# Optimization experiments

Hardware: AMD Instinct MI355X
Metric: run time of the kernel (lower is better)

The kernel has to match this reference:

```python
import jax, jax.numpy as jnp
import numpy as np
import math

STD = math.exp(0.0025)  # exp(0.5 * 0.005) from log_sigma = 0.005
C = 0.5 * math.log(2 * math.pi)
B, X, H, Z, L, W = 8192, 512, 256, 64, 16, 32

def _predict(h, Wd, bd, Wo, bo):
    return jax.nn.sigmoid(jax.nn.relu(h @ Wd.T + bd) @ Wo.T + bo)

def _gru(xin, h, Wih, Whh, bih, bhh):
    gi = xin @ Wih.T + bih
    gh = h @ Whh.T + bhh
    ir, iz, inn = jnp.split(gi, 3, axis=1)
    hr, hz, hn = jnp.split(gh, 3, axis=1)
    r = jax.nn.sigmoid(ir + hr)
    zt = jax.nn.sigmoid(iz + hz)
    n = jnp.tanh(inn + r * hn)
    return (1.0 - zt) * n + zt * h

def setup_inputs():
    key = jax.random.key(0)
    ks = iter(jax.random.split(key, 40))
    def nrm(shape, s=0.05):
        return jax.random.normal(next(ks), shape, dtype=jnp.float32) * s
    return {
        "x": jax.random.uniform(next(ks), (B, X), dtype=jnp.float32),
        "workers": jax.random.uniform(next(ks), (W, B, L), dtype=jnp.float32),
        "Wf1": nrm((H, X)), "bf1": jnp.zeros((H,)),
        "Wf2": nrm((1, H)), "bf2": jnp.zeros((1,)),
        "eWih": nrm((L, 3 * H, X + 1)), "eWhh": nrm((L, 3 * H, H)),
        "ebih": jnp.zeros((L, 3 * H)), "ebhh": jnp.zeros((L, 3 * H)),
        "eWd": nrm((L, H, H)), "ebd": jnp.zeros((L, H)),
        "eWo": nrm((L, 1, H)), "ebo": jnp.zeros((L, 1)),
        "Wmu": nrm((Z, H)), "bmu": jnp.zeros((Z,)),
        "Wlv": nrm((Z, H)), "blv": jnp.zeros((Z,)),
        "dWih": nrm((L, 3 * H, Z + 1)), "dWhh": nrm((L, 3 * H, H)),
        "dbih": jnp.zeros((L, 3 * H)), "dbhh": jnp.zeros((L, 3 * H)),
        "dWd": nrm((L, H, H)), "dbd": jnp.zeros((L, H)),
        "dWo": nrm((L, W, H)), "dbo": jnp.zeros((L, W)),
        "Wr": nrm((X, H)), "br": jnp.zeros((X,)),
        "enc_eps": jax.random.normal(next(ks), (L, B, H), dtype=jnp.float32),
        "samp_eps": jax.random.normal(next(ks), (B, Z), dtype=jnp.float32),
        "dec_eps": jax.random.uniform(next(ks), (L, B, H), dtype=jnp.float32),
    }

def _forward(x, workers, Wf1, bf1, Wf2, bf2, eWih, eWhh, ebih, ebhh, eWd, ebd, eWo, ebo,
             Wmu, bmu, Wlv, blv, dWih, dWhh, dbih, dbhh, dWd, dbd, dWo, dbo, Wr, br,
             enc_eps, samp_eps, dec_eps):
    nB = x.shape[0]
    h_dim = eWhh.shape[2]
    # Encoder: t[:,0] = firstcell(x)
    t0 = _predict(x, Wf1, bf1, Wf2, bf2)[:, 0]
    z0 = jnp.zeros((nB, h_dim), dtype=x.dtype)

    def enc_step(carry, xs):
        z, ti = carry
        Wih, Whh, bih, bhh, Wd, bd, Wo, bo, eps = xs
        tmp = (ti >= 0.5).astype(x.dtype)
        mu = _gru(jnp.concatenate([x, tmp[:, None]], axis=1), z, Wih, Whh, bih, bhh)
        znew = mu + STD * eps
        tn = _predict(znew, Wd, bd, Wo, bo)[:, 0]
        return (znew, tn), ti

    (z_fin, _), tcols = jax.lax.scan(
        enc_step, (z0, t0), (eWih, eWhh, ebih, ebhh, eWd, ebd, eWo, ebo, enc_eps))
    t = tcols.T  # [B, L]
    mu_z = z_fin @ Wmu.T + bmu
    log_var = jax.nn.softplus(z_fin @ Wlv.T + blv)
    latent = mu_z + jnp.exp(0.5 * log_var) * samp_eps
    tmp_t = (t > 0.5).astype(x.dtype)

    def dec_step(zt, xs):
        Wih, Whh, bih, bhh, Wd, bd, Wo, bo, tcol, eps = xs
        mu = _gru(jnp.concatenate([latent, tcol[:, None]], axis=1), zt, Wih, Whh, bih, bhh)
        znew = mu + STD * eps  # decoder uses uniform eps (torch.rand)
        return znew, _predict(znew, Wd, bd, Wo, bo)

    zT, preds = jax.lax.scan(
        dec_step, jnp.zeros((nB, h_dim), dtype=x.dtype),
        (dWih, dWhh, dbih, dbhh, dWd, dbd, dWo, dbo, tmp_t.T, dec_eps))
    worker_preds = jnp.transpose(preds, (2, 1, 0))  # [L,B,W] -> [W,B,L]
    recon = jax.nn.sigmoid(zT @ Wr.T + br)
    log_p_x = jnp.sum(x * jnp.log(recon), axis=1)
    logp = jnp.clip(jnp.log(worker_preds), -100.0)
    log1mp = jnp.clip(jnp.log1p(-worker_preds), -100.0)
    bce = -(workers * logp + (1.0 - workers) * log1mp)
    log_p_y = -jnp.sum(jnp.sum(bce, axis=0), axis=1)
    workers_bar = jnp.mean(workers, axis=0)
    log_kl = jnp.sum(t * (jnp.log(t + 1e-6) - jnp.log(workers_bar + 1e-6)), axis=1)
    log_p_z = jnp.sum(-C - latent ** 2 / 2, axis=-1)
    log_q = jnp.sum(-C - log_var / 2 - (latent - mu_z) ** 2 / (2 * jnp.exp(log_var)), axis=-1)
    loss = jnp.mean(log_q - log_p_z - log_p_y - log_p_x + log_kl)
    return t, loss

def reference(x, workers, Wf1, bf1, Wf2, bf2, eWih, eWhh, ebih, ebhh, eWd, ebd, eWo, ebo,
              Wmu, bmu, Wlv, blv, dWih, dWhh, dbih, dbhh, dWd, dbd, dWo, dbo, Wr, br,
              enc_eps, samp_eps, dec_eps):
    return _forward(x, workers, Wf1, bf1, Wf2, bf2, eWih, eWhh, ebih, ebhh, eWd, ebd,
                    eWo, ebo, Wmu, bmu, Wlv, blv, dWih, dWhh, dbih, dbhh, dWd, dbd,
                    dWo, dbo, Wr, br, enc_eps, samp_eps, dec_eps)
```

## Files before the change

kernel.cpp:

```cpp
#include <hip/hip_runtime.h>
#include <hip/hip_bf16.h>
#include <math.h>

#define B_ 8192
#define X_ 512
#define H_ 256
#define Z_ 64
#define L_ 16
#define W_ 32
#define G3_ 768

#define STDF 1.0025031276057952f
#define CC 0.9189385332046727f

typedef _Float16 f16x8 __attribute__((ext_vector_type(8)));
typedef float f32x4 __attribute__((ext_vector_type(4)));

__device__ __forceinline__ float sigm(float x) { return 1.0f / (1.0f + expf(-x)); }
__device__ __forceinline__ float logsig(float u) {
    return (u > 0.0f) ? -log1pf(expf(-u)) : (u - log1pf(expf(u)));
}

#define GLOAD16(gsrc, ldst) \
    __builtin_amdgcn_global_load_lds((const __attribute__((address_space(1))) unsigned int*)(gsrc), \
                                     (__attribute__((address_space(3))) unsigned int*)(ldst), 16, 0, 0)

template<int BN>
__global__ __launch_bounds__(256) void mfma_gemm(
    const _Float16* __restrict__ A,
    const _Float16* __restrict__ Wt,
    const float* __restrict__ bias,
    float* __restrict__ C, int ldc,
    int K, int act)
{
    constexpr int BM = 128;
    constexpr int WN = BN / 2;
    constexpr int NFR = WN / 16;
    __shared__ char smem[(BM + BN) * 128];
    char* Asmem = smem;
    char* Wsmem = smem + BM * 128;

    const int tid  = threadIdx.x;
    const int wave = tid >> 6;
    const int lane = tid & 63;
    const int wr   = wave >> 1;
    const int wc   = wave & 1;
    const int bm   = blockIdx.y * BM;
    const int bn   = blockIdx.x * BN;
    const int l15  = lane & 15;
    const int l4   = lane >> 4;

    f32x4 acc[4][NFR];
    #pragma unroll
    for (int a = 0; a < 4; ++a)
        #pragma unroll
        for (int b = 0; b < NFR; ++b) {
            f32x4 zz = {0.f, 0.f, 0.f, 0.f};
            acc[a][b] = zz;
        }

    for (int k0 = 0; k0 < K; k0 += 64) {
        #pragma unroll
        for (int it = 0; it < 4; ++it) {
            int o   = (it * 4 + wave) * 1024 + lane * 16;
            int row = o >> 7;
            int c   = ((o >> 4) & 7) ^ (row & 7);
            GLOAD16(A + (long)(bm + row) * K + k0 + c * 8, Asmem + (it * 4 + wave) * 1024);
        }
        #pragma unroll
        for (int it = 0; it < BN / 32; ++it) {
            int o   = (it * 4 + wave) * 1024 + lane * 16;
            int row = o >> 7;
            int c   = ((o >> 4) & 7) ^ (row & 7);
            GLOAD16(Wt + (long)(bn + row) * K + k0 + c * 8, Wsmem + (it * 4 + wave) * 1024);
        }
        asm volatile("s_waitcnt vmcnt(0)" ::: "memory");
        __syncthreads();
        #pragma unroll
        for (int ks = 0; ks < 2; ++ks) {
            f16x8 af[4], bf[NFR];
            #pragma unroll
            for (int mi = 0; mi < 4; ++mi) {
                int row = wr * 64 + mi * 16 + l15;
                int c   = (ks * 4 + l4) ^ (row & 7);
                af[mi] = *(const f16x8*)(Asmem + row * 128 + c * 16);
            }
            #pragma unroll
            for (int ni = 0; ni < NFR; ++ni) {
                int row = wc * WN + ni * 16 + l15;
                int c   = (ks * 4 + l4) ^ (row & 7);
                bf[ni] = *(const f16x8*)(Wsmem + row * 128 + c * 16);
            }
            #pragma unroll
            for (int mi = 0; mi < 4; ++mi)
                #pragma unroll
                for (int ni = 0; ni < NFR; ++ni)
                    acc[mi][ni] = __builtin_amdgcn_mfma_f32_16x16x32_f16(
                        af[mi], bf[ni], acc[mi][ni], 0, 0, 0);
        }
        __syncthreads();
    }

    #pragma unroll
    for (int mi = 0; mi < 4; ++mi)
        #pragma unroll
        for (int r = 0; r < 4; ++r) {
            int grow = bm + wr * 64 + mi * 16 + l4 * 4 + r;
            #pragma unroll
            for (int ni = 0; ni < NFR; ++ni) {
                int gcol = bn + wc * WN + ni * 16 + l15;
                float v = acc[mi][ni][r] + bias[gcol];
                if (act) v = fmaxf(v, 0.0f);
                C[(long)grow * ldc + gcol] = v;
            }
        }
}

template<int MODE, int KX>
__global__ __launch_bounds__(256) void gru_fused(
    const _Float16* __restrict__ A2,
    const _Float16* __restrict__ Wih,
    const float* __restrict__ bih,
    const _Float16* __restrict__ Whh,
    const float* __restrict__ bhh,
    const float* __restrict__ ec,
    const float* __restrict__ tcol,
    const float* __restrict__ eps,
    const _Float16* __restrict__ zh_in,
    float* __restrict__ z,
    _Float16* __restrict__ zh_out)
{
    __shared__ char smem[(64 + 192) * 128];
    char* Asmem = smem;
    char* Wsmem = smem + 64 * 128;

    const int tid  = threadIdx.x;
    const int wave = tid >> 6;
    const int lane = tid & 63;
    const int wr   = wave >> 1;
    const int wc   = wave & 1;
    const int id   = blockIdx.x;
    const int xcd  = id & 7;
    const int wk   = id >> 3;
    const int bm   = (xcd * 16 + (wk >> 2)) * 64;
    const int h0   = (wk & 3) * 64;
    const int l15  = lane & 15;
    const int l4   = lane >> 4;

    f32x4 acc[2][6];
    f32x4 accN[2][2];
    #pragma unroll
    for (int a = 0; a < 2; ++a) {
        #pragma unroll
        for (int b = 0; b < 6; ++b) { f32x4 zz = {0.f,0.f,0.f,0.f}; acc[a][b] = zz; }
        #pragma unroll
        for (int b = 0; b < 2; ++b) { f32x4 zz = {0.f,0.f,0.f,0.f}; accN[a][b] = zz; }
    }

    for (int k0 = 0; k0 < KX; k0 += 64) {
        #pragma unroll
        for (int it = 0; it < 2; ++it) {
            int q   = it * 4 + wave;
            int o   = q * 1024 + lane * 16;
            int row = o >> 7;
            int c   = ((o >> 4) & 7) ^ (row & 7);
            GLOAD16(A2 + (long)(bm + row) * KX + k0 + c * 8, Asmem + q * 1024);
        }
        #pragma unroll
        for (int it = 0; it < 6; ++it) {
            int q   = it * 4 + wave;
            int o   = q * 1024 + lane * 16;
            int rr  = o >> 7;
            int c   = ((o >> 4) & 7) ^ (rr & 7);
            int srow = (rr >> 6) * 256 + h0 + (rr & 63);
            GLOAD16(Wih + (long)srow * KX + k0 + c * 8, Wsmem + q * 1024);
        }
        asm volatile("s_waitcnt vmcnt(0)" ::: "memory");
        __syncthreads();
        #pragma unroll
        for (int ks = 0; ks < 2; ++ks) {
            f16x8 af[2], bf[6];
            #pragma unroll
            for (int mi = 0; mi < 2; ++mi) {
                int row = wr * 32 + mi * 16 + l15;
                int c   = (ks * 4 + l4) ^ (row & 7);
                af[mi] = *(const f16x8*)(Asmem + row * 128 + c * 16);
            }
            #pragma unroll
            for (int ni = 0; ni < 6; ++ni) {
                int rr = (ni >> 1) * 64 + wc * 32 + (ni & 1) * 16 + l15;
                int c  = (ks * 4 + l4) ^ (rr & 7);
                bf[ni] = *(const f16x8*)(Wsmem + rr * 128 + c * 16);
            }
            #pragma unroll
            for (int mi = 0; mi < 2; ++mi) {
                #pragma unroll
                for (int ni = 0; ni < 4; ++ni)
                    acc[mi][ni] = __builtin_amdgcn_mfma_f32_16x16x32_f16(
                        af[mi], bf[ni], acc[mi][ni], 0, 0, 0);
                #pragma unroll
                for (int ni = 4; ni < 6; ++ni)
                    accN[mi][ni - 4] = __builtin_amdgcn_mfma_f32_16x16x32_f16(
                        af[mi], bf[ni], accN[mi][ni - 4], 0, 0, 0);
            }
        }
        __syncthreads();
    }

    for (int k0 = 0; k0 < 256; k0 += 64) {
        #pragma unroll
        for (int it = 0; it < 2; ++it) {
            int q   = it * 4 + wave;
            int o   = q * 1024 + lane * 16;
            int row = o >> 7;
            int c   = ((o >> 4) & 7) ^ (row & 7);
            GLOAD16(zh_in + (long)(bm + row) * 256 + k0 + c * 8, Asmem + q * 1024);
        }
        #pragma unroll
        for (int it = 0; it < 6; ++it) {
            int q   = it * 4 + wave;
            int o   = q * 1024 + lane * 16;
            int rr  = o >> 7;
            int c   = ((o >> 4) & 7) ^ (rr & 7);
            int srow = (rr >> 6) * 256 + h0 + (rr & 63);
            GLOAD16(Whh + (long)srow * 256 + k0 + c * 8, Wsmem + q * 1024);
        }
        asm volatile("s_waitcnt vmcnt(0)" ::: "memory");
        __syncthreads();
        #pragma unroll
        for (int ks = 0; ks < 2; ++ks) {
            f16x8 af[2], bf[6];
            #pragma unroll
            for (int mi = 0; mi < 2; ++mi) {
                int row = wr * 32 + mi * 16 + l15;
                int c   = (ks * 4 + l4) ^ (row & 7);
                af[mi] = *(const f16x8*)(Asmem + row * 128 + c * 16);
            }
            #pragma unroll
            for (int ni = 0; ni < 6; ++ni) {
                int rr = (ni >> 1) * 64 + wc * 32 + (ni & 1) * 16 + l15;
                int c  = (ks * 4 + l4) ^ (rr & 7);
                bf[ni] = *(const f16x8*)(Wsmem + rr * 128 + c * 16);
            }
            #pragma unroll
            for (int mi = 0; mi < 2; ++mi)
                #pragma unroll
                for (int ni = 0; ni < 6; ++ni)
                    acc[mi][ni] = __builtin_amdgcn_mfma_f32_16x16x32_f16(
                        af[mi], bf[ni], acc[mi][ni], 0, 0, 0);
        }
        __syncthreads();
    }

    #pragma unroll
    for (int mi = 0; mi < 2; ++mi)
        #pragma unroll
        for (int r = 0; r < 4; ++r) {
            int grow = bm + wr * 32 + mi * 16 + l4 * 4 + r;
            float tv = tcol[(long)grow * L_];
            float ext = (MODE == 1) ? (tv >= 0.5f ? 1.0f : 0.0f)
                                    : (tv >  0.5f ? 1.0f : 0.0f);
            #pragma unroll
            for (int hb = 0; hb < 2; ++hb) {
                int h = h0 + wc * 32 + hb * 16 + l15;
                float rpre = acc[mi][hb][r]     + bih[h]       + bhh[h]       + ext * ec[h];
                float zpre = acc[mi][2 + hb][r] + bih[256 + h] + bhh[256 + h] + ext * ec[256 + h];
                float hn   = acc[mi][4 + hb][r] + bhh[512 + h];
                float in_  = accN[mi][hb][r]    + bih[512 + h] + ext * ec[512 + h];
                float rg = sigm(rpre);
                float zt = sigm(zpre);
                float n  = tanhf(in_ + rg * hn);
                long zi = (long)grow * 256 + h;
                float v = (1.0f - zt) * n + zt * z[zi] + STDF * eps[zi];
                z[zi] = v;
                zh_out[zi] = (_Float16)v;
            }
        }
}

__global__ __launch_bounds__(256) void predict_head(
    const _Float16* __restrict__ A, int K,
    const _Float16* __restrict__ Wd,
    const float* __restrict__ bd,
    const float* __restrict__ wo,
    const float* __restrict__ bo,
    float* __restrict__ out, int ostride)
{
    __shared__ char smem[(32 + 256) * 128];
    __shared__ float part[32][4];
    char* Asmem = smem;
    char* Wsmem = smem + 32 * 128;

    const int tid  = threadIdx.x;
    const int wave = tid >> 6;
    const int lane = tid & 63;
    const int bm   = blockIdx.x * 32;
    const int l15  = lane & 15;
    const int l4   = lane >> 4;

    f32x4 acc[2][4];
    #pragma unroll
    for (int a = 0; a < 2; ++a)
        #pragma unroll
        for (int b = 0; b < 4; ++b) { f32x4 zz = {0.f,0.f,0.f,0.f}; acc[a][b] = zz; }

    for (int k0 = 0; k0 < K; k0 += 64) {
        {
            int o   = wave * 1024 + lane * 16;
            int row = o >> 7;
            int c   = ((o >> 4) & 7) ^ (row & 7);
            GLOAD16(A + (long)(bm + row) * K + k0 + c * 8, Asmem + wave * 1024);
        }
        #pragma unroll
        for (int it = 0; it < 8; ++it) {
            int q   = it * 4 + wave;
            int o   = q * 1024 + lane * 16;
            int row = o >> 7;
            int c   = ((o >> 4) & 7) ^ (row & 7);
            GLOAD16(Wd + (long)row * K + k0 + c * 8, Wsmem + q * 1024);
        }
        asm volatile("s_waitcnt vmcnt(0)" ::: "memory");
        __syncthreads();
        #pragma unroll
        for (int ks = 0; ks < 2; ++ks) {
            f16x8 af[2], bf[4];
            #pragma unroll
            for (int mi = 0; mi < 2; ++mi) {
                int row = mi * 16 + l15;
                int c   = (ks * 4 + l4) ^ (row & 7);
                af[mi] = *(const f16x8*)(Asmem + row * 128 + c * 16);
            }
            #pragma unroll
            for (int ni = 0; ni < 4; ++ni) {
                int row = wave * 64 + ni * 16 + l15;
                int c   = (ks * 4 + l4) ^ (row & 7);
                bf[ni] = *(const f16x8*)(Wsmem + row * 128 + c * 16);
            }
            #pragma unroll
            for (int mi = 0; mi < 2; ++mi)
                #pragma unroll
                for (int ni = 0; ni < 4; ++ni)
                    acc[mi][ni] = __builtin_amdgcn_mfma_f32_16x16x32_f16(
                        af[mi], bf[ni], acc[mi][ni], 0, 0, 0);
        }
        __syncthreads();
    }

    float bdv[4], wov[4];
    #pragma unroll
    for (int ni = 0; ni < 4; ++ni) {
        int col = wave * 64 + ni * 16 + l15;
        bdv[ni] = bd[col];
        wov[ni] = wo[col];
    }
    #pragma unroll
    for (int mi = 0; mi < 2; ++mi)
        #pragma unroll
        for (int r = 0; r < 4; ++r) {
            float s = 0.0f;
            #pragma unroll
            for (int ni = 0; ni < 4; ++ni) {
                float v = fmaxf(acc[mi][ni][r] + bdv[ni], 0.0f);
                s = fmaf(v, wov[ni], s);
            }
            #pragma unroll
            for (int off = 1; off < 16; off <<= 1) s += __shfl_xor(s, off, 16);
            if (l15 == 0) part[mi * 16 + l4 * 4 + r][wave] = s;
        }
    __syncthreads();
    if (tid < 32) {
        float u = part[tid][0] + part[tid][1] + part[tid][2] + part[tid][3] + bo[0];
        out[(long)(bm + tid) * ostride] = sigm(u);
    }
}

__global__ __launch_bounds__(256) void dec_head_bce(
    const _Float16* __restrict__ A,
    const _Float16* __restrict__ Wd,
    const float* __restrict__ bd,
    const _Float16* __restrict__ Wo,
    const float* __restrict__ bo,
    const float* __restrict__ wt,
    float* __restrict__ bacc)
{
    __shared__ char smem[(32 + 256) * 128];
    __shared__ _Float16 ds[32 * 264];
    __shared__ float part[32][2];
    char* Asmem = smem;
    char* Wsmem = smem + 32 * 128;

    const int tid  = threadIdx.x;
    const int wave = tid >> 6;
    const int lane = tid & 63;
    const int bm   = blockIdx.x * 32;
    const int l15  = lane & 15;
    const int l4   = lane >> 4;

    f32x4 acc[2][4];
    #pragma unroll
    for (int a = 0; a < 2; ++a)
        #pragma unroll
        for (int b = 0; b < 4; ++b) { f32x4 zz = {0.f,0.f,0.f,0.f}; acc[a][b] = zz; }

    for (int k0 = 0; k0 < 256; k0 += 64) {
        {
            int o   = wave * 1024 + lane * 16;
            int row = o >> 7;
            int c   = ((o >> 4) & 7) ^ (row & 7);
            GLOAD16(A + (long)(bm + row) * 256 + k0 + c * 8, Asmem + wave * 1024);
        }
        #pragma unroll
        for (int it = 0; it < 8; ++it) {
            int q   = it * 4 + wave;
            int o   = q * 1024 + lane * 16;
            int row = o >> 7;
            int c   = ((o >> 4) & 7) ^ (row & 7);
            GLOAD16(Wd + (long)row * 256 + k0 + c * 8, Wsmem + q * 1024);
        }
        asm volatile("s_waitcnt vmcnt(0)" ::: "memory");
        __syncthreads();
        #pragma unroll
        for (int ks = 0; ks < 2; ++ks) {
            f16x8 af[2], bf[4];
            #pragma unroll
            for (int mi = 0; mi < 2; ++mi) {
                int row = mi * 16 + l15;
                int c   = (ks * 4 + l4) ^ (row & 7);
                af[mi] = *(const f16x8*)(Asmem + row * 128 + c * 16);
            }
            #pragma unroll
            for (int ni = 0; ni < 4; ++ni) {
                int row = wave * 64 + ni * 16 + l15;
                int c   = (ks * 4 + l4) ^ (row & 7);
                bf[ni] = *(const f16x8*)(Wsmem + row * 128 + c * 16);
            }
            #pragma unroll
            for (int mi = 0; mi < 2; ++mi)
                #pragma unroll
                for (int ni = 0; ni < 4; ++ni)
                    acc[mi][ni] = __builtin_amdgcn_mfma_f32_16x16x32_f16(
                        af[mi], bf[ni], acc[mi][ni], 0, 0, 0);
        }
        __syncthreads();
    }

    #pragma unroll
    for (int mi = 0; mi < 2; ++mi)
        #pragma unroll
        for (int r = 0; r < 4; ++r) {
            int row = mi * 16 + l4 * 4 + r;
            #pragma unroll
            for (int ni = 0; ni < 4; ++ni) {
                int col = wave * 64 + ni * 16 + l15;
                ds[row * 264 + col] = (_Float16)fmaxf(acc[mi][ni][r] + bd[col], 0.0f);
            }
        }
    __syncthreads();

    const int rh = wave >> 1;
    const int ch = wave & 1;
    f32x4 acc2 = {0.f, 0.f, 0.f, 0.f};
    #pragma unroll
    for (int k = 0; k < 8; ++k) {
        f16x8 bf2 = *(const f16x8*)(Wo + (long)(ch * 16 + l15) * 256 + k * 32 + l4 * 8);
        f16x8 af  = *(const f16x8*)(ds + (rh * 16 + l15) * 264 + k * 32 + l4 * 8);
        acc2 = __builtin_amdgcn_mfma_f32_16x16x32_f16(af, bf2, acc2, 0, 0, 0);
    }

    #pragma unroll
    for (int r = 0; r < 4; ++r) {
        int row = rh * 16 + l4 * 4 + r;
        int w = ch * 16 + l15;
        float u = acc2[r] + bo[w];
        float logp   = fmaxf(logsig(u),  -100.0f);
        float log1mp = fmaxf(logsig(-u), -100.0f);
        float wk = wt[(long)(bm + row) * W_ + w];
        float s = -(wk * logp + (1.0f - wk) * log1mp);
        #pragma unroll
        for (int off = 1; off < 16; off <<= 1) s += __shfl_xor(s, off, 16);
        if (l15 == 0) part[row][ch] = s;
    }
    __syncthreads();
    if (tid < 32) bacc[bm + tid] += part[tid][0] + part[tid][1];
}

__global__ __launch_bounds__(256) void wtrans(
    const float* __restrict__ workers, float* __restrict__ wt)
{
    long idx = (long)blockIdx.x * 256 + threadIdx.x;
    int w = idx & 31;
    long b = idx >> 5;
    const float* src = workers + (w * (long)B_ + b) * L_;
    #pragma unroll
    for (int l = 0; l < L_; ++l)
        wt[((long)l * B_ + b) * W_ + w] = src[l];
}

struct ConvJobs {
    const float* s[10];
    _Float16* d[10];
};
__device__ __constant__ const long CJ_CNT[10] = {
    (long)B_ * X_,
    (long)H_ * X_,
    (long)L_ * G3_ * H_,
    (long)L_ * H_ * H_,
    (long)L_ * G3_ * H_,
    (long)L_ * H_ * H_,
    (long)L_ * W_ * H_,
    (long)X_ * H_,
    (long)Z_ * H_,
    (long)Z_ * H_
};
#define CJ_TOTAL 13008896L

__global__ __launch_bounds__(256) void conv_multi(ConvJobs J)
{
    long i8 = ((long)blockIdx.x * 256 + threadIdx.x) * 8;
    if (i8 >= CJ_TOTAL) return;
    long rem = i8; int j = 0;
    #pragma unroll
    for (int k = 0; k < 9; ++k)
        if (rem >= CJ_CNT[k]) { rem -= CJ_CNT[k]; ++j; } else break;
    const float* s = J.s[j] + rem;
    f16x8 o;
    #pragma unroll
    for (int q = 0; q < 8; ++q) o[q] = (_Float16)s[q];
    *(f16x8*)(J.d[j] + rem) = o;
}

__global__ __launch_bounds__(256) void conv_f16(
    const float* __restrict__ src, _Float16* __restrict__ dst,
    int Ks, int Kd, long total)
{
    long i = ((long)blockIdx.x * 256 + threadIdx.x) * 8;
    if (i >= total) return;
    long r = i / Kd, k = i - r * Kd;
    const float* s = src + r * Ks + k;
    f16x8 o;
    #pragma unroll
    for (int j = 0; j < 8; ++j) o[j] = (_Float16)s[j];
    *(f16x8*)(dst + i) = o;
}

__global__ __launch_bounds__(256) void extract_col(
    const float* __restrict__ src, float* __restrict__ dst, int Ks, int col, int R)
{
    int i = blockIdx.x * 256 + threadIdx.x;
    if (i < R) dst[i] = src[(long)i * Ks + col];
}

__global__ void stack_bias(const float* __restrict__ a, const float* __restrict__ b,
                           float* __restrict__ o)
{
    int i = threadIdx.x;
    o[i] = (i < 64) ? a[i] : b[i - 64];
}

__global__ __launch_bounds__(256) void zero2_kernel(
    float* __restrict__ z, _Float16* __restrict__ zh, int n)
{
    int i = blockIdx.x * 256 + threadIdx.x;
    if (i < n) { z[i] = 0.0f; zh[i] = (_Float16)0.0f; }
}

__global__ __launch_bounds__(256) void zero_kernel(float* __restrict__ p, int n)
{
    int i = blockIdx.x * 256 + threadIdx.x;
    if (i < n) p[i] = 0.0f;
}

__global__ __launch_bounds__(256) void latent_elem(
    const float* __restrict__ muv,
    const float* __restrict__ seps,
    float* __restrict__ latent, _Float16* __restrict__ lath,
    float* __restrict__ lq, float* __restrict__ lpz)
{
    int wave = threadIdx.x >> 6, lane = threadIdx.x & 63;
    int b = blockIdx.x * 4 + wave;
    float mu = muv[(long)b * 128 + lane];
    float sp = muv[(long)b * 128 + 64 + lane];
    float lv = (sp > 0.0f) ? (sp + log1pf(expf(-sp))) : log1pf(expf(sp));
    float e  = seps[(long)b * Z_ + lane];
    float lat = mu + expf(0.5f * lv) * e;
    latent[(long)b * Z_ + lane] = lat;
    lath[(long)b * Z_ + lane] = (_Float16)lat;
    float lpz_c = -CC - 0.5f * lat * lat;
    float d = lat - mu;
    float lq_c = -CC - 0.5f * lv - d * d / (2.0f * expf(lv));
    #pragma unroll
    for (int off = 32; off; off >>= 1) {
        lpz_c += __shfl_down(lpz_c, off);
        lq_c  += __shfl_down(lq_c, off);
    }
    if (lane == 0) { lpz[b] = lpz_c; lq[b] = lq_c; }
}

__global__ __launch_bounds__(256) void logpx_reduce(
    const float* __restrict__ u, const float* __restrict__ x,
    float* __restrict__ lpx)
{
    int wave = threadIdx.x >> 6, lane = threadIdx.x & 63;
    int b = blockIdx.x * 4 + wave;
    const float* ub = u + (long)b * X_;
    const float* xb = x + (long)b * X_;
    float s = 0.0f;
    #pragma unroll
    for (int i = 0; i < 8; ++i) {
        int k = lane + i * 64;
        s = fmaf(xb[k], logsig(ub[k]), s);
    }
    #pragma unroll
    for (int off = 32; off; off >>= 1) s += __shfl_down(s, off);
    if (lane == 0) lpx[b] = s;
}

__global__ __launch_bounds__(256) void kl_kernel(
    const float* __restrict__ tmat, const float* __restrict__ workers,
    float* __restrict__ lkl)
{
    int b = blockIdx.x * 256 + threadIdx.x;
    float wb[L_];
    #pragma unroll
    for (int l = 0; l < L_; ++l) wb[l] = 0.0f;
    for (int w = 0; w < W_; ++w) {
        const float* p = workers + ((long)w * B_ + b) * L_;
        #pragma unroll
        for (int l = 0; l < L_; ++l) wb[l] += p[l];
    }
    float s = 0.0f;
    #pragma unroll
    for (int l = 0; l < L_; ++l) {
        float wbar = wb[l] * (1.0f / 32.0f);
        float tv = tmat[(long)b * L_ + l];
        s += tv * (logf(tv + 1e-6f) - logf(wbar + 1e-6f));
    }
    lkl[b] = s;
}

__global__ __launch_bounds__(1024) void final_reduce(
    const float* __restrict__ lq, const float* __restrict__ lpz,
    const float* __restrict__ bacc, const float* __restrict__ lpx,
    const float* __restrict__ lkl, float* __restrict__ out)
{
    __shared__ float red[16];
    float s = 0.0f;
    for (int b = threadIdx.x; b < B_; b += 1024)
        s += lq[b] - lpz[b] + bacc[b] - lpx[b] + lkl[b];
    #pragma unroll
    for (int off = 32; off; off >>= 1) s += __shfl_down(s, off);
    int wave = threadIdx.x >> 6, lane = threadIdx.x & 63;
    if (lane == 0) red[wave] = s;
    __syncthreads();
    if (threadIdx.x == 0) {
        float t = 0.0f;
        for (int i = 0; i < 16; ++i) t += red[i];
        out[0] = t / (float)B_;
    }
}

extern "C" void kernel_launch(void* const* d_in, const int* in_sizes, int n_in,
                              void* d_out, int out_size, void* d_ws, size_t ws_size,
                              hipStream_t stream)
{
    const float* x       = (const float*)d_in[0];
    const float* workers = (const float*)d_in[1];
    const float* Wf1     = (const float*)d_in[2];
    const float* bf1     = (const float*)d_in[3];
    const float* Wf2     = (const float*)d_in[4];
    const float* bf2     = (const float*)d_in[5];
    const float* eWih    = (const float*)d_in[6];
    const float* eWhh    = (const float*)d_in[7];
    const float* ebih    = (const float*)d_in[8];
    const float* ebhh    = (const float*)d_in[9];
    const float* eWd     = (const float*)d_in[10];
    const float* ebd     = (const float*)d_in[11];
    const float* eWo     = (const float*)d_in[12];
    const float* ebo     = (const float*)d_in[13];
    const float* Wmu     = (const float*)d_in[14];
    const float* bmu     = (const float*)d_in[15];
    const float* Wlv     = (const float*)d_in[16];
    const float* blv     = (const float*)d_in[17];
    const float* dWih    = (const float*)d_in[18];
    const float* dWhh    = (const float*)d_in[19];
    const float* dbih    = (const float*)d_in[20];
    const float* dbhh    = (const float*)d_in[21];
    const float* dWd     = (const float*)d_in[22];
    const float* dbd     = (const float*)d_in[23];
    const float* dWo     = (const float*)d_in[24];
    const float* dbo     = (const float*)d_in[25];
    const float* Wr      = (const float*)d_in[26];
    const float* br      = (const float*)d_in[27];
    const float* enc_eps = (const float*)d_in[28];
    const float* samp_eps= (const float*)d_in[29];
    const float* dec_eps = (const float*)d_in[30];

    float* t    = (float*)d_out;
    float* loss = t + (long)B_ * L_;

    char* p = (char*)d_ws;
    auto alloc = [&](size_t bytes) {
        char* r = p;
        p += (bytes + 255) & ~(size_t)255;
        return r;
    };
    _Float16* xh    = (_Float16*)alloc((size_t)B_ * X_ * 2);
    _Float16* zha   = (_Float16*)alloc((size_t)B_ * H_ * 2);
    _Float16* zhb   = (_Float16*)alloc((size_t)B_ * H_ * 2);
    _Float16* lath  = (_Float16*)alloc((size_t)B_ * Z_ * 2);
    _Float16* Wf1h  = (_Float16*)alloc((size_t)H_ * X_ * 2);
    _Float16* eWihh = (_Float16*)alloc((size_t)L_ * G3_ * X_ * 2);
    _Float16* eWhhh = (_Float16*)alloc((size_t)L_ * G3_ * H_ * 2);
    _Float16* eWdh  = (_Float16*)alloc((size_t)L_ * H_ * H_ * 2);
    _Float16* dWihh = (_Float16*)alloc((size_t)L_ * G3_ * Z_ * 2);
    _Float16* dWhhh = (_Float16*)alloc((size_t)L_ * G3_ * H_ * 2);
    _Float16* dWdh  = (_Float16*)alloc((size_t)L_ * H_ * H_ * 2);
    _Float16* dWoh  = (_Float16*)alloc((size_t)L_ * W_ * H_ * 2);
    _Float16* Wrh   = (_Float16*)alloc((size_t)X_ * H_ * 2);
    _Float16* Wmlh  = (_Float16*)alloc((size_t)128 * H_ * 2);
    float* bml    = (float*)alloc(128 * 4);
    float* eWihc  = (float*)alloc((size_t)L_ * G3_ * 4);
    float* dWihc  = (float*)alloc((size_t)L_ * G3_ * 4);
    float* z      = (float*)alloc((size_t)B_ * H_ * 4);
    float* dbuf   = (float*)alloc((size_t)B_ * H_ * 4);
    float* latent = (float*)alloc((size_t)B_ * Z_ * 4);
    float* wt     = (float*)alloc((size_t)L_ * B_ * W_ * 4);
    float* logits = (float*)alloc((size_t)B_ * X_ * 4);
    float* lq     = (float*)alloc((size_t)B_ * 4);
    float* lpz    = (float*)alloc((size_t)B_ * 4);
    float* lpx    = (float*)alloc((size_t)B_ * 4);
    float* lkl    = (float*)alloc((size_t)B_ * 4);
    float* bacc   = (float*)alloc((size_t)B_ * 4);

    const dim3 blk(256);
    const int nBH = B_ * H_;
    auto cgrid = [](long total) { return dim3((unsigned)((total / 8 + 255) / 256)); };

    ConvJobs J;
    J.s[0] = x;    J.d[0] = xh;
    J.s[1] = Wf1;  J.d[1] = Wf1h;
    J.s[2] = eWhh; J.d[2] = eWhhh;
    J.s[3] = eWd;  J.d[3] = eWdh;
    J.s[4] = dWhh; J.d[4] = dWhhh;
    J.s[5] = dWd;  J.d[5] = dWdh;
    J.s[6] = dWo;  J.d[6] = dWoh;
    J.s[7] = Wr;   J.d[7] = Wrh;
    J.s[8] = Wmu;  J.d[8] = Wmlh;
    J.s[9] = Wlv;  J.d[9] = Wmlh + (long)Z_ * H_;
    conv_multi<<<(CJ_TOTAL / 8 + 255) / 256, blk, 0, stream>>>(J);
    conv_f16<<<cgrid((long)L_ * G3_ * X_), blk, 0, stream>>>(eWih, eWihh, X_ + 1, X_, (long)L_ * G3_ * X_);
    conv_f16<<<cgrid((long)L_ * G3_ * Z_), blk, 0, stream>>>(dWih, dWihh, Z_ + 1, Z_, (long)L_ * G3_ * Z_);
    stack_bias<<<1, 128, 0, stream>>>(bmu, blv, bml);
    extract_col<<<(L_ * G3_ + 255) / 256, blk, 0, stream>>>(eWih, eWihc, X_ + 1, X_, L_ * G3_);
    extract_col<<<(L_ * G3_ + 255) / 256, blk, 0, stream>>>(dWih, dWihc, Z_ + 1, Z_, L_ * G3_);
    wtrans<<<(W_ * B_) / 256, blk, 0, stream>>>(workers, wt);

    zero2_kernel<<<(nBH + 255) / 256, blk, 0, stream>>>(z, zha, nBH);
    predict_head<<<B_ / 32, blk, 0, stream>>>(xh, X_, Wf1h, bf1, Wf2, bf2, t, L_);

    _Float16* zcur = zha;
    _Float16* znxt = zhb;
    for (int l = 0; l < L_; ++l) {
        gru_fused<1, X_><<<512, blk, 0, stream>>>(
            xh, eWihh + (long)l * G3_ * X_, ebih + (long)l * G3_,
            eWhhh + (long)l * G3_ * H_, ebhh + (long)l * G3_,
            eWihc + (long)l * G3_, t + l, enc_eps + (long)l * nBH,
            zcur, z, znxt);
        _Float16* tmp = zcur; zcur = znxt; znxt = tmp;
        if (l < L_ - 1)
            predict_head<<<B_ / 32, blk, 0, stream>>>(
                zcur, H_, eWdh + (long)l * H_ * H_, ebd + (long)l * H_,
                eWo + (long)l * H_, ebo + l, t + (l + 1), L_);
    }

    mfma_gemm<64><<<dim3(2, B_ / 128), blk, 0, stream>>>(
        zcur, Wmlh, bml, dbuf, 128, H_, 0);
    latent_elem<<<B_ / 4, blk, 0, stream>>>(dbuf, samp_eps, latent, lath, lq, lpz);

    zero2_kernel<<<(nBH + 255) / 256, blk, 0, stream>>>(z, zha, nBH);
    zero_kernel<<<(B_ + 255) / 256, blk, 0, stream>>>(bacc, B_);
    zcur = zha; znxt = zhb;
    for (int l = 0; l < L_; ++l) {
        gru_fused<2, Z_><<<512, blk, 0, stream>>>(
            lath, dWihh + (long)l * G3_ * Z_, dbih + (long)l * G3_,
            dWhhh + (long)l * G3_ * H_, dbhh + (long)l * G3_,
            dWihc + (long)l * G3_, t + l, dec_eps + (long)l * nBH,
            zcur, z, znxt);
        _Float16* tmp = zcur; zcur = znxt; znxt = tmp;
        dec_head_bce<<<B_ / 32, blk, 0, stream>>>(
            zcur, dWdh + (long)l * H_ * H_, dbd + (long)l * H_,
            dWoh + (long)l * W_ * H_, dbo + (long)l * W_,
            wt + (long)l * B_ * W_, bacc);
    }

    mfma_gemm<128><<<dim3(X_ / 128, B_ / 128), blk, 0, stream>>>(
        zcur, Wrh, br, logits, X_, H_, 0);
    logpx_reduce<<<B_ / 4, blk, 0, stream>>>(logits, x, lpx);
    kl_kernel<<<B_ / 256, blk, 0, stream>>>(t, workers, lkl);
    final_reduce<<<1, 1024, 0, stream>>>(lq, lpz, bacc, lpx, lkl, loss);
}
```

Before: 1.171 ms.

## Double-buffer LDS tiles in GEMM/GRU kernels and skip zero-state hidden matmul

Each MFMA kernel (gemm, gru_fused, predict_head, dec_head_bce) now keeps two LDS buffers, so the global-to-LDS load of the next K tile is issued before computing the current one, with partial vmcnt waits and raw s_barrier. The GRU kernel merges its input and hidden K loops into one pipelined stage sequence. A FIRST template variant skips the hidden-state matmul and the old-z read at step zero, since the state is zero there, and the zeroing kernels are removed, with the bacc reset folded into wtrans. The cost is doubled LDS per block, which may reduce occupancy, and the correctness of the hand-counted vmcnt values.

```diff
diff --git a/kernel.cpp b/kernel.cpp
--- a/kernel.cpp
+++ b/kernel.cpp
@@ -25,6 +25,9 @@
     __builtin_amdgcn_global_load_lds((const __attribute__((address_space(1))) unsigned int*)(gsrc), \
                                      (__attribute__((address_space(3))) unsigned int*)(ldst), 16, 0, 0)
 
+#define WAITV(N) asm volatile("s_waitcnt vmcnt(" #N ")" ::: "memory")
+#define SBAR()  do { __builtin_amdgcn_sched_barrier(0); __builtin_amdgcn_s_barrier(); } while (0)
+
 template<int BN>
 __global__ __launch_bounds__(256) void mfma_gemm(
     const _Float16* __restrict__ A,
@@ -36,9 +39,7 @@
     constexpr int BM = 128;
     constexpr int WN = BN / 2;
     constexpr int NFR = WN / 16;
-    __shared__ char smem[(BM + BN) * 128];
-    char* Asmem = smem;
-    char* Wsmem = smem + BM * 128;
+    __shared__ char smem[2][(BM + BN) * 128];
 
     const int tid  = threadIdx.x;
     const int wave = tid >> 6;
@@ -59,23 +60,39 @@
             acc[a][b] = zz;
         }
 
-    for (int k0 = 0; k0 < K; k0 += 64) {
+    auto stage = [&](int s, int pb) {
+        char* As = smem[pb];
+        char* Ws = smem[pb] + BM * 128;
+        int k0 = s * 64;
         #pragma unroll
         for (int it = 0; it < 4; ++it) {
-            int o   = (it * 4 + wave) * 1024 + lane * 16;
+            int q   = it * 4 + wave;
+            int o   = q * 1024 + lane * 16;
             int row = o >> 7;
             int c   = ((o >> 4) & 7) ^ (row & 7);
-            GLOAD16(A + (long)(bm + row) * K + k0 + c * 8, Asmem + (it * 4 + wave) * 1024);
+            GLOAD16(A + (long)(bm + row) * K + k0 + c * 8, As + q * 1024);
         }
         #pragma unroll
         for (int it = 0; it < BN / 32; ++it) {
-            int o   = (it * 4 + wave) * 1024 + lane * 16;
+            int q   = it * 4 + wave;
+            int o   = q * 1024 + lane * 16;
             int row = o >> 7;
             int c   = ((o >> 4) & 7) ^ (row & 7);
-            GLOAD16(Wt + (long)(bn + row) * K + k0 + c * 8, Wsmem + (it * 4 + wave) * 1024);
-        }
-        asm volatile("s_waitcnt vmcnt(0)" ::: "memory");
-        __syncthreads();
+            GLOAD16(Wt + (long)(bn + row) * K + k0 + c * 8, Ws + q * 1024);
+        }
+    };
+
+    const int NT = K >> 6;
+    stage(0, 0);
+    for (int s = 0; s < NT; ++s) {
+        int pb = s & 1;
+        if (s + 1 < NT) {
+            stage(s + 1, pb ^ 1);
+            if constexpr (BN == 128) WAITV(8); else WAITV(6);
+        } else WAITV(0);
+        SBAR();
+        char* As = smem[pb];
+        char* Ws = smem[pb] + BM * 128;
         #pragma unroll
         for (int ks = 0; ks < 2; ++ks) {
             f16x8 af[4], bf[NFR];
@@ -83,13 +100,13 @@
             for (int mi = 0; mi < 4; ++mi) {
                 int row = wr * 64 + mi * 16 + l15;
                 int c   = (ks * 4 + l4) ^ (row & 7);
-                af[mi] = *(const f16x8*)(Asmem + row * 128 + c * 16);
+                af[mi] = *(const f16x8*)(As + row * 128 + c * 16);
             }
             #pragma unroll
             for (int ni = 0; ni < NFR; ++ni) {
                 int row = wc * WN + ni * 16 + l15;
                 int c   = (ks * 4 + l4) ^ (row & 7);
-                bf[ni] = *(const f16x8*)(Wsmem + row * 128 + c * 16);
+                bf[ni] = *(const f16x8*)(Ws + row * 128 + c * 16);
             }
             #pragma unroll
             for (int mi = 0; mi < 4; ++mi)
@@ -98,7 +115,7 @@
                     acc[mi][ni] = __builtin_amdgcn_mfma_f32_16x16x32_f16(
                         af[mi], bf[ni], acc[mi][ni], 0, 0, 0);
         }
-        __syncthreads();
+        SBAR();
     }
 
     #pragma unroll
@@ -116,7 +133,7 @@
         }
 }
 
-template<int MODE, int KX>
+template<int MODE, int KX, int FIRST>
 __global__ __launch_bounds__(256) void gru_fused(
     const _Float16* __restrict__ A2,
     const _Float16* __restrict__ Wih,
@@ -130,9 +147,9 @@
     float* __restrict__ z,
     _Float16* __restrict__ zh_out)
 {
-    __shared__ char smem[(64 + 192) * 128];
-    char* Asmem = smem;
-    char* Wsmem = smem + 64 * 128;
+    constexpr int N1 = KX / 64;
+    constexpr int NT = N1 + (FIRST ? 0 : 4);
+    __shared__ char smem[2][(64 + 192) * 128];
 
     const int tid  = threadIdx.x;
     const int wave = tid >> 6;
@@ -157,14 +174,21 @@
         for (int b = 0; b < 2; ++b) { f32x4 zz = {0.f,0.f,0.f,0.f}; accN[a][b] = zz; }
     }
 
-    for (int k0 = 0; k0 < KX; k0 += 64) {
+    auto stage = [&](int s, int pb) {
+        char* As = smem[pb];
+        char* Ws = smem[pb] + 64 * 128;
+        const _Float16* srcA;
+        const _Float16* srcW;
+        int KA, k0;
+        if (s < N1) { srcA = A2;    srcW = Wih; KA = KX;  k0 = s * 64; }
+        else        { srcA = zh_in; srcW = Whh; KA = 256; k0 = (s - N1) * 64; }
         #pragma unroll
         for (int it = 0; it < 2; ++it) {
             int q   = it * 4 + wave;
             int o   = q * 1024 + lane * 16;
             int row = o >> 7;
             int c   = ((o >> 4) & 7) ^ (row & 7);
-            GLOAD16(A2 + (long)(bm + row) * KX + k0 + c * 8, Asmem + q * 1024);
+            GLOAD16(srcA + (long)(bm + row) * KA + k0 + c * 8, As + q * 1024);
         }
         #pragma unroll
         for (int it = 0; it < 6; ++it) {
@@ -173,10 +197,19 @@
             int rr  = o >> 7;
             int c   = ((o >> 4) & 7) ^ (rr & 7);
             int srow = (rr >> 6) * 256 + h0 + (rr & 63);
-            GLOAD16(Wih + (long)srow * KX + k0 + c * 8, Wsmem + q * 1024);
-        }
-        asm volatile("s_waitcnt vmcnt(0)" ::: "memory");
-        __syncthreads();
+            GLOAD16(srcW + (long)srow * KA + k0 + c * 8, Ws + q * 1024);
+        }
+    };
+
+    stage(0, 0);
+    for (int s = 0; s < NT; ++s) {
+        int pb = s & 1;
+        if (s + 1 < NT) { stage(s + 1, pb ^ 1); WAITV(8); }
+        else WAITV(0);
+        SBAR();
+        char* As = smem[pb];
+        char* Ws = smem[pb] + 64 * 128;
+        bool p1 = (s < N1);
         #pragma unroll
         for (int ks = 0; ks < 2; ++ks) {
             f16x8 af[2], bf[6];
@@ -184,72 +217,36 @@
             for (int mi = 0; mi < 2; ++mi) {
                 int row = wr * 32 + mi * 16 + l15;
                 int c   = (ks * 4 + l4) ^ (row & 7);
-                af[mi] = *(const f16x8*)(Asmem + row * 128 + c * 16);
+                af[mi] = *(const f16x8*)(As + row * 128 + c * 16);
             }
             #pragma unroll
             for (int ni = 0; ni < 6; ++ni) {
                 int rr = (ni >> 1) * 64 + wc * 32 + (ni & 1) * 16 + l15;
                 int c  = (ks * 4 + l4) ^ (rr & 7);
-                bf[ni] = *(const f16x8*)(Wsmem + rr * 128 + c * 16);
-            }
-            #pragma unroll
-            for (int mi = 0; mi < 2; ++mi) {
+                bf[ni] = *(const f16x8*)(Ws + rr * 128 + c * 16);
+            }
+            if (p1) {
                 #pragma unroll
-                for (int ni = 0; ni < 4; ++ni)
-                    acc[mi][ni] = __builtin_amdgcn_mfma_f32_16x16x32_f16(
-                        af[mi], bf[ni], acc[mi][ni], 0, 0, 0);
+                for (int mi = 0; mi < 2; ++mi) {
+                    #pragma unroll
+                    for (int ni = 0; ni < 4; ++ni)
+                        acc[mi][ni] = __builtin_amdgcn_mfma_f32_16x16x32_f16(
+                            af[mi], bf[ni], acc[mi][ni], 0, 0, 0);
+                    #pragma unroll
+                    for (int ni = 4; ni < 6; ++ni)
+                        accN[mi][ni - 4] = __builtin_amdgcn_mfma_f32_16x16x32_f16(
+                            af[mi], bf[ni], accN[mi][ni - 4], 0, 0, 0);
+                }
+            } else {
                 #pragma unroll
-                for (int ni = 4; ni < 6; ++ni)
-                    accN[mi][ni - 4] = __builtin_amdgcn_mfma_f32_16x16x32_f16(
-                        af[mi], bf[ni], accN[mi][ni - 4], 0, 0, 0);
-            }
-        }
-        __syncthreads();
-    }
-
-    for (int k0 = 0; k0 < 256; k0 += 64) {
-        #pragma unroll
-        for (int it = 0; it < 2; ++it) {
-            int q   = it * 4 + wave;
-            int o   = q * 1024 + lane * 16;
-            int row = o >> 7;
-            int c   = ((o >> 4) & 7) ^ (row & 7);
-            GLOAD16(zh_in + (long)(bm + row) * 256 + k0 + c * 8, Asmem + q * 1024);
-        }
-        #pragma unroll
-        for (int it = 0; it < 6; ++it) {
-            int q   = it * 4 + wave;
-            int o   = q * 1024 + lane * 16;
-            int rr  = o >> 7;
-            int c   = ((o >> 4) & 7) ^ (rr & 7);
-            int srow = (rr >> 6) * 256 + h0 + (rr & 63);
-            GLOAD16(Whh + (long)srow * 256 + k0 + c * 8, Wsmem + q * 1024);
-        }
-        asm volatile("s_waitcnt vmcnt(0)" ::: "memory");
-        __syncthreads();
-        #pragma unroll
-        for (int ks = 0; ks < 2; ++ks) {
-            f16x8 af[2], bf[6];
-            #pragma unroll
-            for (int mi = 0; mi < 2; ++mi) {
-                int row = wr * 32 + mi * 16 + l15;
-                int c   = (ks * 4 + l4) ^ (row & 7);
-                af[mi] = *(const f16x8*)(Asmem + row * 128 + c * 16);
-            }
-            #pragma unroll
-            for (int ni = 0; ni < 6; ++ni) {
-                int rr = (ni >> 1) * 64 + wc * 32 + (ni & 1) * 16 + l15;
-                int c  = (ks * 4 + l4) ^ (rr & 7);
-                bf[ni] = *(const f16x8*)(Wsmem + rr * 128 + c * 16);
-            }
-            #pragma unroll
-            for (int mi = 0; mi < 2; ++mi)
-                #pragma unroll
-                for (int ni = 0; ni < 6; ++ni)
-                    acc[mi][ni] = __builtin_amdgcn_mfma_f32_16x16x32_f16(
-                        af[mi], bf[ni], acc[mi][ni], 0, 0, 0);
-        }
-        __syncthreads();
+                for (int mi = 0; mi < 2; ++mi)
+                    #pragma unroll
+                    for (int ni = 0; ni < 6; ++ni)
+                        acc[mi][ni] = __builtin_amdgcn_mfma_f32_16x16x32_f16(
+                            af[mi], bf[ni], acc[mi][ni], 0, 0, 0);
+            }
+        }
+        SBAR();
     }
 
     #pragma unroll
@@ -271,25 +268,26 @@
                 float zt = sigm(zpre);
                 float n  = tanhf(in_ + rg * hn);
                 long zi = (long)grow * 256 + h;
-                float v = (1.0f - zt) * n + zt * z[zi] + STDF * eps[zi];
+                float zold = FIRST ? 0.0f : z[zi];
+                float v = (1.0f - zt) * n + zt * zold + STDF * eps[zi];
                 z[zi] = v;
                 zh_out[zi] = (_Float16)v;
             }
         }
 }
 
+template<int K>
 __global__ __launch_bounds__(256) void predict_head(
-    const _Float16* __restrict__ A, int K,
+    const _Float16* __restrict__ A,
     const _Float16* __restrict__ Wd,
     const float* __restrict__ bd,
     const float* __restrict__ wo,
     const float* __restrict__ bo,
     float* __restrict__ out, int ostride)
 {
-    __shared__ char smem[(32 + 256) * 128];
+    constexpr int NT = K / 64;
+    __shared__ char smem[2][(32 + 256) * 128];
     __shared__ float part[32][4];
-    char* Asmem = smem;
-    char* Wsmem = smem + 32 * 128;
 
     const int tid  = threadIdx.x;
     const int wave = tid >> 6;
@@ -304,12 +302,15 @@
         #pragma unroll
         for (int b = 0; b < 4; ++b) { f32x4 zz = {0.f,0.f,0.f,0.f}; acc[a][b] = zz; }
 
-    for (int k0 = 0; k0 < K; k0 += 64) {
+    auto stage = [&](int s, int pb) {
+        char* As = smem[pb];
+        char* Ws = smem[pb] + 32 * 128;
+        int k0 = s * 64;
         {
             int o   = wave * 1024 + lane * 16;
             int row = o >> 7;
             int c   = ((o >> 4) & 7) ^ (row & 7);
-            GLOAD16(A + (long)(bm + row) * K + k0 + c * 8, Asmem + wave * 1024);
+            GLOAD16(A + (long)(bm + row) * K + k0 + c * 8, As + wave * 1024);
         }
         #pragma unroll
         for (int it = 0; it < 8; ++it) {
@@ -317,10 +318,18 @@
             int o   = q * 1024 + lane * 16;
             int row = o >> 7;
             int c   = ((o >> 4) & 7) ^ (row & 7);
-            GLOAD16(Wd + (long)row * K + k0 + c * 8, Wsmem + q * 1024);
-        }
-        asm volatile("s_waitcnt vmcnt(0)" ::: "memory");
-        __syncthreads();
+            GLOAD16(Wd + (long)row * K + k0 + c * 8, Ws + q * 1024);
+        }
+    };
+
+    stage(0, 0);
+    for (int s = 0; s < NT; ++s) {
+        int pb = s & 1;
+        if (s + 1 < NT) { stage(s + 1, pb ^ 1); WAITV(9); }
+        else WAITV(0);
+        SBAR();
+        char* As = smem[pb];
+        char* Ws = smem[pb] + 32 * 128;
         #pragma unroll
         for (int ks = 0; ks < 2; ++ks) {
             f16x8 af[2], bf[4];
@@ -328,13 +337,13 @@
             for (int mi = 0; mi < 2; ++mi) {
                 int row = mi * 16 + l15;
                 int c   = (ks * 4 + l4) ^ (row & 7);
-                af[mi] = *(const f16x8*)(Asmem + row * 128 + c * 16);
+                af[mi] = *(const f16x8*)(As + row * 128 + c * 16);
             }
             #pragma unroll
             for (int ni = 0; ni < 4; ++ni) {
                 int row = wave * 64 + ni * 16 + l15;
                 int c   = (ks * 4 + l4) ^ (row & 7);
-                bf[ni] = *(const f16x8*)(Wsmem + row * 128 + c * 16);
+                bf[ni] = *(const f16x8*)(Ws + row * 128 + c * 16);
             }
             #pragma unroll
             for (int mi = 0; mi < 2; ++mi)
@@ -343,7 +352,7 @@
                     acc[mi][ni] = __builtin_amdgcn_mfma_f32_16x16x32_f16(
                         af[mi], bf[ni], acc[mi][ni], 0, 0, 0);
         }
-        __syncthreads();
+        SBAR();
     }
 
     float bdv[4], wov[4];
@@ -383,11 +392,10 @@
     const float* __restrict__ wt,
     float* __restrict__ bacc)
 {
-    __shared__ char smem[(32 + 256) * 128];
+    constexpr int NT = 4;
+    __shared__ char smem[2][(32 + 256) * 128];
     __shared__ _Float16 ds[32 * 264];
     __shared__ float part[32][2];
-    char* Asmem = smem;
-    char* Wsmem = smem + 32 * 128;
 
     const int tid  = threadIdx.x;
     const int wave = tid >> 6;
@@ -402,12 +410,15 @@
         #pragma unroll
         for (int b = 0; b < 4; ++b) { f32x4 zz = {0.f,0.f,0.f,0.f}; acc[a][b] = zz; }
 
-    for (int k0 = 0; k0 < 256; k0 += 64) {
+    auto stage = [&](int s, int pb) {
+        char* As = smem[pb];
+        char* Ws = smem[pb] + 32 * 128;
+        int k0 = s * 64;
         {
             int o   = wave * 1024 + lane * 16;
             int row = o >> 7;
             int c   = ((o >> 4) & 7) ^ (row & 7);
-            GLOAD16(A + (long)(bm + row) * 256 + k0 + c * 8, Asmem + wave * 1024);
+            GLOAD16(A + (long)(bm + row) * 256 + k0 + c * 8, As + wave * 1024);
         }
         #pragma unroll
         for (int it = 0; it < 8; ++it) {
@@ -415,10 +426,18 @@
             int o   = q * 1024 + lane * 16;
             int row = o >> 7;
             int c   = ((o >> 4) & 7) ^ (row & 7);
-            GLOAD16(Wd + (long)row * 256 + k0 + c * 8, Wsmem + q * 1024);
-        }
-        asm volatile("s_waitcnt vmcnt(0)" ::: "memory");
-        __syncthreads();
+            GLOAD16(Wd + (long)row * 256 + k0 + c * 8, Ws + q * 1024);
+        }
+    };
+
+    stage(0, 0);
+    for (int s = 0; s < NT; ++s) {
+        int pb = s & 1;
+        if (s + 1 < NT) { stage(s + 1, pb ^ 1); WAITV(9); }
+        else WAITV(0);
+        SBAR();
+        char* As = smem[pb];
+        char* Ws = smem[pb] + 32 * 128;
         #pragma unroll
         for (int ks = 0; ks < 2; ++ks) {
             f16x8 af[2], bf[4];
@@ -426,13 +445,13 @@
             for (int mi = 0; mi < 2; ++mi) {
                 int row = mi * 16 + l15;
                 int c   = (ks * 4 + l4) ^ (row & 7);
-                af[mi] = *(const f16x8*)(Asmem + row * 128 + c * 16);
+                af[mi] = *(const f16x8*)(As + row * 128 + c * 16);
             }
             #pragma unroll
             for (int ni = 0; ni < 4; ++ni) {
                 int row = wave * 64 + ni * 16 + l15;
                 int c   = (ks * 4 + l4) ^ (row & 7);
-                bf[ni] = *(const f16x8*)(Wsmem + row * 128 + c * 16);
+                bf[ni] = *(const f16x8*)(Ws + row * 128 + c * 16);
             }
             #pragma unroll
             for (int mi = 0; mi < 2; ++mi)
@@ -441,7 +460,7 @@
                     acc[mi][ni] = __builtin_amdgcn_mfma_f32_16x16x32_f16(
                         af[mi], bf[ni], acc[mi][ni], 0, 0, 0);
         }
-        __syncthreads();
+        SBAR();
     }
 
     #pragma unroll
@@ -485,7 +504,8 @@
 }
 
 __global__ __launch_bounds__(256) void wtrans(
-    const float* __restrict__ workers, float* __restrict__ wt)
+    const float* __restrict__ workers, float* __restrict__ wt,
+    float* __restrict__ bacc)
 {
     long idx = (long)blockIdx.x * 256 + threadIdx.x;
     int w = idx & 31;
@@ -494,6 +514,7 @@
     #pragma unroll
     for (int l = 0; l < L_; ++l)
         wt[((long)l * B_ + b) * W_ + w] = src[l];
+    if (w == 0) bacc[b] = 0.0f;
 }
 
 struct ConvJobs {
@@ -555,19 +576,6 @@
 {
     int i = threadIdx.x;
     o[i] = (i < 64) ? a[i] : b[i - 64];
-}
-
-__global__ __launch_bounds__(256) void zero2_kernel(
-    float* __restrict__ z, _Float16* __restrict__ zh, int n)
-{
-    int i = blockIdx.x * 256 + threadIdx.x;
-    if (i < n) { z[i] = 0.0f; zh[i] = (_Float16)0.0f; }
-}
-
-__global__ __launch_bounds__(256) void zero_kernel(float* __restrict__ p, int n)
-{
-    int i = blockIdx.x * 256 + threadIdx.x;
-    if (i < n) p[i] = 0.0f;
 }
 
 __global__ __launch_bounds__(256) void latent_elem(
@@ -753,23 +761,26 @@
     stack_bias<<<1, 128, 0, stream>>>(bmu, blv, bml);
     extract_col<<<(L_ * G3_ + 255) / 256, blk, 0, stream>>>(eWih, eWihc, X_ + 1, X_, L_ * G3_);
     extract_col<<<(L_ * G3_ + 255) / 256, blk, 0, stream>>>(dWih, dWihc, Z_ + 1, Z_, L_ * G3_);
-    wtrans<<<(W_ * B_) / 256, blk, 0, stream>>>(workers, wt);
-
-    zero2_kernel<<<(nBH + 255) / 256, blk, 0, stream>>>(z, zha, nBH);
-    predict_head<<<B_ / 32, blk, 0, stream>>>(xh, X_, Wf1h, bf1, Wf2, bf2, t, L_);
+    wtrans<<<(W_ * B_) / 256, blk, 0, stream>>>(workers, wt, bacc);
+
+    predict_head<X_><<<B_ / 32, blk, 0, stream>>>(xh, Wf1h, bf1, Wf2, bf2, t, L_);
 
     _Float16* zcur = zha;
     _Float16* znxt = zhb;
     for (int l = 0; l < L_; ++l) {
-        gru_fused<1, X_><<<512, blk, 0, stream>>>(
-            xh, eWihh + (long)l * G3_ * X_, ebih + (long)l * G3_,
-            eWhhh + (long)l * G3_ * H_, ebhh + (long)l * G3_,
-            eWihc + (long)l * G3_, t + l, enc_eps + (long)l * nBH,
-            zcur, z, znxt);
+        if (l == 0)
+            gru_fused<1, X_, 1><<<512, blk, 0, stream>>>(
+                xh, eWihh, ebih, eWhhh, ebhh, eWihc, t, enc_eps, zcur, z, znxt);
+        else
+            gru_fused<1, X_, 0><<<512, blk, 0, stream>>>(
+                xh, eWihh + (long)l * G3_ * X_, ebih + (long)l * G3_,
+                eWhhh + (long)l * G3_ * H_, ebhh + (long)l * G3_,
+                eWihc + (long)l * G3_, t + l, enc_eps + (long)l * nBH,
+                zcur, z, znxt);
         _Float16* tmp = zcur; zcur = znxt; znxt = tmp;
         if (l < L_ - 1)
-            predict_head<<<B_ / 32, blk, 0, stream>>>(
-                zcur, H_, eWdh + (long)l * H_ * H_, ebd + (long)l * H_,
+            predict_head<H_><<<B_ / 32, blk, 0, stream>>>(
+                zcur, eWdh + (long)l * H_ * H_, ebd + (long)l * H_,
                 eWo + (long)l * H_, ebo + l, t + (l + 1), L_);
     }
 
@@ -777,15 +788,17 @@
         zcur, Wmlh, bml, dbuf, 128, H_, 0);
     latent_elem<<<B_ / 4, blk, 0, stream>>>(dbuf, samp_eps, latent, lath, lq, lpz);
 
-    zero2_kernel<<<(nBH + 255) / 256, blk, 0, stream>>>(z, zha, nBH);
-    zero_kernel<<<(B_ + 255) / 256, blk, 0, stream>>>(bacc, B_);
     zcur = zha; znxt = zhb;
     for (int l = 0; l < L_; ++l) {
-        gru_fused<2, Z_><<<512, blk, 0, stream>>>(
-            lath, dWihh + (long)l * G3_ * Z_, dbih + (long)l * G3_,
-            dWhhh + (long)l * G3_ * H_, dbhh + (long)l * G3_,
-            dWihc + (long)l * G3_, t + l, dec_eps + (long)l * nBH,
-            zcur, z, znxt);
+        if (l == 0)
+            gru_fused<2, Z_, 1><<<512, blk, 0, stream>>>(
+                lath, dWihh, dbih, dWhhh, dbhh, dWihc, t, dec_eps, zcur, z, znxt);
+        else
+            gru_fused<2, Z_, 0><<<512, blk, 0, stream>>>(
+                lath, dWihh + (long)l * G3_ * Z_, dbih + (long)l * G3_,
+                dWhhh + (long)l * G3_ * H_, dbhh + (long)l * G3_,
+                dWihc + (long)l * G3_, t + l, dec_eps + (long)l * nBH,
+                zcur, z, znxt);
         _Float16* tmp = zcur; zcur = znxt; znxt = tmp;
         dec_head_bce<<<B_ / 32, blk, 0, stream>>>(
             zcur, dWdh + (long)l * H_ * H_, dbd + (long)l * H_,
```

Measured after the change: 1.107 ms. -5.5%, faster.
